# Optimization experiments

Measured on AMD Instinct MI355X. Metric: run time of the kernel, lower is better.

The kernel has to match this reference:

```python
import jax, jax.numpy as jnp
import numpy as np

NA, NW, H = 20000, 100000, 128
DA, DW = 64, 128
E_CR, E_IN, E_CO = 400000, 600000, 300000


def _seg_softmax(logits, seg, n):
    m = jax.ops.segment_max(logits, seg, num_segments=n)
    e = jnp.exp(logits - m[seg])
    s = jax.ops.segment_sum(e, seg, num_segments=n)
    return e / (s[seg] + 1e-16)


def _gat(x_src, x_dst, edge, W, b, a_s, a_d):
    # PyG GATConv, heads=1, concat=False, shared lin for src/dst, add_self_loops=True
    n_src, n_dst = x_src.shape[0], x_dst.shape[0]
    loops = jnp.arange(min(n_src, n_dst), dtype=edge.dtype)
    src = jnp.concatenate([edge[0], loops])
    dst = jnp.concatenate([edge[1], loops])
    hs = x_src @ W            # [n_src, H]
    hd = x_dst @ W            # [n_dst, H]
    logit = jax.nn.leaky_relu((hs @ a_s)[src] + (hd @ a_d)[dst], 0.2)
    alpha = _seg_softmax(logit, dst, n_dst)          # softmax over in-neighborhoods
    out = jax.ops.segment_sum(alpha[:, None] * hs[src], dst, num_segments=n_dst)
    return out + b


def _mlp2(x, w1, b1, w2, b2):
    return jax.nn.relu(x @ w1 + b1) @ w2 + b2


def setup_inputs() -> dict:
    key = jax.random.key(0)
    ks = iter(jax.random.split(key, 40))

    def p(shape, scale=0.1):
        return jax.random.normal(next(ks), shape, jnp.float32) * scale

    def edges(n_src, n_dst, E):
        s = jax.random.randint(next(ks), (E,), 0, n_src, dtype=jnp.int32)
        d = jax.random.randint(next(ks), (E,), 0, n_dst, dtype=jnp.int32)
        d = jnp.where(s == d, (d + 1) % n_dst, d)  # keep input loop-free (PyG strips them)
        return jnp.stack([s, d])

    e_creates = edges(NA, NW, E_CR)
    inp = {
        'artist_feat': jax.random.normal(next(ks), (NA, DA), jnp.float32),
        'work_feat': jax.random.normal(next(ks), (NW, DW), jnp.float32),
        'a_w1': p((DA, H)), 'a_b1': jnp.zeros(H, jnp.float32),
        'a_w2': p((H, H)), 'a_b2': jnp.zeros(H, jnp.float32),
        'w_w1': p((DW, H)), 'w_b1': jnp.zeros(H, jnp.float32),
        'w_w2': p((H, H)), 'w_b2': jnp.zeros(H, jnp.float32),
        'cr_W': p((H, H)), 'cr_b': jnp.zeros(H, jnp.float32), 'cr_as': p((H,)), 'cr_ad': p((H,)),
        'in_W': p((H, H)), 'in_b': jnp.zeros(H, jnp.float32), 'in_as': p((H,)), 'in_ad': p((H,)),
        'co_W': p((H, H)), 'co_b': jnp.zeros(H, jnp.float32), 'co_as': p((H,)), 'co_ad': p((H,)),
        'p_w1': p((2 * H, 256)), 'p_b1': jnp.zeros(256, jnp.float32),
        'p_w2': p((256, 128)), 'p_b2': jnp.zeros(128, jnp.float32),
        'p_w3': p((128, 1)), 'p_b3': jnp.zeros(1, jnp.float32),
        'e_creates': e_creates,
        'e_created_by': jnp.flip(e_creates, axis=0),  # reverse relation [work, artist]
        'e_infl': edges(NW, NW, E_IN),
        'e_collab': edges(NA, NA, E_CO),
    }
    return inp


def reference(artist_feat, work_feat,
              a_w1, a_b1, a_w2, a_b2,
              w_w1, w_b1, w_w2, w_b2,
              cr_W, cr_b, cr_as, cr_ad,
              in_W, in_b, in_as, in_ad,
              co_W, co_b, co_as, co_ad,
              p_w1, p_b1, p_w2, p_b2, p_w3, p_b3,
              e_creates, e_created_by, e_infl, e_collab):
    ax = _mlp2(artist_feat, a_w1, a_b1, a_w2, a_b2)      # [NA, H]
    wx = _mlp2(work_feat, w_w1, w_b1, w_w2, w_b2)        # [NW, H]
    wx = jax.nn.elu(_gat(ax, wx, e_creates, cr_W, cr_b, cr_as, cr_ad))
    wx = jax.nn.elu(_gat(wx, wx, e_infl, in_W, in_b, in_as, in_ad))
    au = _gat(wx, ax, e_created_by, cr_W, cr_b, cr_as, cr_ad)  # no elu (matches source)
    ac = jax.nn.elu(_gat(au, au, e_collab, co_W, co_b, co_as, co_ad))
    comb = jnp.concatenate([au, ac], axis=1)             # [NA, 2H]
    h = jax.nn.relu(comb @ p_w1 + p_b1)                  # dropout is identity in eval
    h = jax.nn.relu(h @ p_w2 + p_b2)
    return (h @ p_w3 + p_b3).squeeze()
```

## Files before the change

### kernel.cpp

```cpp
#include <hip/hip_runtime.h>
#include <hip/hip_bf16.h>
#include <cstddef>

#define NA 20000
#define NW 100000
#define HH 128
#define DA 64
#define E_CR 400000
#define E_IN 600000
#define E_CO 300000

#define ROW1 0
#define ROW2 (NW)
#define ROW3 (2 * NW)
#define ROW4 (2 * NW + NA)
#define NTOT (2 * NW + 2 * NA)
#define T1 (E_CR + NA)
#define T2 (E_IN + NW)
#define T3 (E_CR + NA)
#define T4 (E_CO + NA)
#define ETOT (T1 + T2 + T3 + T4)
#define CAPW 40
#define CAPA 88

typedef short v8s __attribute__((ext_vector_type(8)));
typedef float v4f __attribute__((ext_vector_type(4)));

constexpr int PSLOT = 2 * 128 * 264;

__device__ inline short f2bf(float x) {
    union { float f; unsigned u; } c; c.f = x;
    unsigned r = c.u + 0x7fff + ((c.u >> 16) & 1);
    return (short)(r >> 16);
}
__device__ inline float bf2f(short s) {
    union { unsigned u; float f; } c; c.u = ((unsigned)(unsigned short)s) << 16;
    return c.f;
}
__device__ inline float bfu2f(unsigned short s) {
    union { unsigned u; float f; } c; c.u = ((unsigned)s) << 16;
    return c.f;
}

__device__ inline void split8(const float* xv, v8s& h, v8s& l) {
#pragma unroll
    for (int p = 0; p < 4; ++p) {
        float2 xf; xf.x = xv[2 * p]; xf.y = xv[2 * p + 1];
        __hip_bfloat162 hb = __float22bfloat162_rn(xf);
        float2 hf = __bfloat1622float2(hb);
        float2 lf; lf.x = xf.x - hf.x; lf.y = xf.y - hf.y;
        __hip_bfloat162 lb = __float22bfloat162_rn(lf);
        union { __hip_bfloat162 b; short2 s; } uh, ul;
        uh.b = hb; ul.b = lb;
        h[2 * p] = uh.s.x; h[2 * p + 1] = uh.s.y;
        l[2 * p] = ul.s.x; l[2 * p + 1] = ul.s.y;
    }
}

struct PrepDesc { const float* src; int ldw; int K; };
struct PrepArgs { PrepDesc d[10]; const float* wvW; const float* wvA; float* vd; };

__global__ __launch_bounds__(256) void k_prep(PrepArgs a, short* __restrict__ out) {
    if (blockIdx.x == 10 * 128) {
        __shared__ float sa[HH];
        int t = threadIdx.x;
        if (t < HH) sa[t] = a.wvA[t];
        __syncthreads();
        if (t < HH) {
            float s = 0.f;
            for (int jj = 0; jj < HH; ++jj) s += a.wvW[(size_t)t * HH + jj] * sa[jj];
            a.vd[t] = s;
        }
        return;
    }
    int m = blockIdx.x >> 7;
    int e = (blockIdx.x & 127) * 256 + threadIdx.x;
    PrepDesc dd = a.d[m];
    int K = dd.K;
    int KP = (K <= 128) ? K + 8 : K;
    if (e >= K * 128) return;
    int n = e & 127, k = e >> 7;
    float x = dd.src[(size_t)k * dd.ldw + n];
    short h = f2bf(x);
    short l = f2bf(x - bf2f(h));
    short* base = out + (size_t)m * PSLOT;
    base[n * KP + k] = h;
    base[128 * KP + n * KP + k] = l;
}

template<int K, int ACT, int NSS, int ST, int LDSB, int OBF, int DUAL>
__global__ __launch_bounds__(256, 2) void k_mfma(
    const float* __restrict__ X, int ldx,
    const short* __restrict__ Wp,
    const float* __restrict__ bias,
    float* __restrict__ Y, int ldy, int M,
    const float* __restrict__ v1, float* __restrict__ ss1,
    const float* __restrict__ v2, float* __restrict__ ss2,
    const float* __restrict__ sb)
{
    constexpr int KF = K / 32;
    constexpr int KP = LDSB ? K + 8 : K;
    __shared__ short Bs[LDSB ? 2 * 128 * (K + 8) : 8];
    const int tid = threadIdx.x;
    const int wave = tid >> 6, lane = tid & 63;
    const int l15 = lane & 15, quad = lane >> 4;
    int bid = blockIdx.x;
    if (DUAL) {
        int g0 = gridDim.x >> 1;
        if (bid >= g0) { bid -= g0; Wp += PSLOT; bias += 128; Y += 128; }
    }
    const int wrow = bid * 128 + wave * 32;

    if (LDSB) {
        const float4* src = (const float4*)Wp;
        float4* dst = (float4*)Bs;
        constexpr int total = 2 * 128 * KP / 8;
        for (int i = tid; i < total; i += 256) dst[i] = src[i];
    }

    v4f acc[2][8];
#pragma unroll
    for (int rf = 0; rf < 2; ++rf)
#pragma unroll
        for (int cf = 0; cf < 8; ++cf) acc[rf][cf] = (v4f){0.f, 0.f, 0.f, 0.f};

    if (LDSB) {
        v8s ah[2][KF], al[2][KF];
#pragma unroll
        for (int rf = 0; rf < 2; ++rf) {
            int r = wrow + rf * 16 + l15; if (r >= M) r = M - 1;
            const float* xp = X + (size_t)r * ldx + quad * 8;
#pragma unroll
            for (int kf = 0; kf < KF; ++kf) {
                float xv[8];
                *(float4*)&xv[0] = *(const float4*)(xp + kf * 32);
                *(float4*)&xv[4] = *(const float4*)(xp + kf * 32 + 4);
                split8(xv, ah[rf][kf], al[rf][kf]);
            }
        }
        __syncthreads();
#pragma unroll
        for (int kf = 0; kf < KF; ++kf) {
#pragma unroll
            for (int cf = 0; cf < 8; ++cf) {
                const short* bp = &Bs[(cf * 16 + l15) * KP + kf * 32 + quad * 8];
                v8s bh = *(const v8s*)bp;
                v8s bl = *(const v8s*)(bp + 128 * KP);
#pragma unroll
                for (int rf = 0; rf < 2; ++rf) {
                    acc[rf][cf] = __builtin_amdgcn_mfma_f32_16x16x32_bf16(al[rf][kf], bh, acc[rf][cf], 0, 0, 0);
                    acc[rf][cf] = __builtin_amdgcn_mfma_f32_16x16x32_bf16(ah[rf][kf], bl, acc[rf][cf], 0, 0, 0);
                    acc[rf][cf] = __builtin_amdgcn_mfma_f32_16x16x32_bf16(ah[rf][kf], bh, acc[rf][cf], 0, 0, 0);
                }
            }
        }
    } else {
        for (int kf = 0; kf < KF; ++kf) {
            v8s ah[2], al[2];
#pragma unroll
            for (int rf = 0; rf < 2; ++rf) {
                int r = wrow + rf * 16 + l15; if (r >= M) r = M - 1;
                const float* xp = X + (size_t)r * ldx + kf * 32 + quad * 8;
                float xv[8];
                *(float4*)&xv[0] = *(const float4*)xp;
                *(float4*)&xv[4] = *(const float4*)(xp + 4);
                split8(xv, ah[rf], al[rf]);
            }
#pragma unroll
            for (int cf = 0; cf < 8; ++cf) {
                const short* bp = Wp + (size_t)(cf * 16 + l15) * K + kf * 32 + quad * 8;
                v8s bh = *(const v8s*)bp;
                v8s bl = *(const v8s*)(bp + 128 * KP);
#pragma unroll
                for (int rf = 0; rf < 2; ++rf) {
                    acc[rf][cf] = __builtin_amdgcn_mfma_f32_16x16x32_bf16(al[rf], bh, acc[rf][cf], 0, 0, 0);
                    acc[rf][cf] = __builtin_amdgcn_mfma_f32_16x16x32_bf16(ah[rf], bl, acc[rf][cf], 0, 0, 0);
                    acc[rf][cf] = __builtin_amdgcn_mfma_f32_16x16x32_bf16(ah[rf], bh, acc[rf][cf], 0, 0, 0);
                }
            }
        }
    }

    float bv[8], v1c[8], v2c[8];
#pragma unroll
    for (int cf = 0; cf < 8; ++cf) {
        int col = cf * 16 + l15;
        bv[cf] = bias ? bias[col] : 0.f;
        if (NSS >= 1) v1c[cf] = v1[col];
        if (NSS >= 2) v2c[cf] = v2[col];
    }
    float sbv = (NSS >= 1 && sb) ? sb[0] : 0.f;

#pragma unroll
    for (int rf = 0; rf < 2; ++rf) {
#pragma unroll
        for (int reg = 0; reg < 4; ++reg) {
            int r = wrow + rf * 16 + quad * 4 + reg;
            if (r >= M) continue;
            float p1 = 0.f, p2 = 0.f;
#pragma unroll
            for (int cf = 0; cf < 8; ++cf) {
                float o = acc[rf][cf][reg] + bv[cf];
                if (ACT == 1) o = o > 0.f ? o : 0.f;
                if (NSS >= 1) p1 = fmaf(o, v1c[cf], p1);
                if (NSS >= 2) p2 = fmaf(o, v2c[cf], p2);
                if (ST) {
                    if (OBF) ((unsigned short*)Y)[(size_t)r * ldy + cf * 16 + l15] = (unsigned short)f2bf(o);
                    else     Y[(size_t)r * ldy + cf * 16 + l15] = o;
                }
            }
            if (NSS >= 1) {
#pragma unroll
                for (int w = 1; w < 16; w <<= 1) {
                    p1 += __shfl_xor(p1, w, 64);
                    if (NSS >= 2) p2 += __shfl_xor(p2, w, 64);
                }
                if (l15 == 0) {
                    ss1[r] = p1 + sbv;
                    if (NSS >= 2) ss2[r] = p2;
                }
            }
        }
    }
}

struct EdgeSets { const int* e[4]; int E[4]; int row[4]; int cum[5]; int* pad[4]; int cap[4]; };

__global__ __launch_bounds__(256) void k_append(EdgeSets es, int* __restrict__ deg)
{
    int b0 = blockIdx.x * 1024 + threadIdx.x;
    int s[4], d[4], g[4]; bool ok[4];
#pragma unroll
    for (int u = 0; u < 4; ++u) {
        int i = b0 + u * 256;
        ok[u] = i < es.cum[4];
        s[u] = 0; d[u] = 0; g[u] = 0;
        if (ok[u]) {
            int gi = (i >= es.cum[1]) + (i >= es.cum[2]) + (i >= es.cum[3]);
            int t = i - es.cum[gi];
            int E = es.E[gi];
            if (t < E) { s[u] = es.e[gi][t]; d[u] = es.e[gi][E + t]; }
            else       { s[u] = t - E;       d[u] = t - E; }
            g[u] = gi;
        }
    }
    int p[4];
#pragma unroll
    for (int u = 0; u < 4; ++u) if (ok[u]) p[u] = atomicAdd(&deg[es.row[g[u]] + d[u]], 1);
#pragma unroll
    for (int u = 0; u < 4; ++u)
        if (ok[u] && p[u] < es.cap[g[u]])
            es.pad[g[u]][(size_t)d[u] * es.cap[g[u]] + p[u]] = s[u];
}

template<int ELU, int U, int CAP>
__global__ __launch_bounds__(256) void k_aggregate(
    const int* __restrict__ deg, const int* __restrict__ esp,
    const unsigned short* __restrict__ hs, const float* __restrict__ ss,
    const float* __restrict__ sd, const float* __restrict__ bias,
    float* __restrict__ out, int ldy, int n)
{
    int lane = threadIdx.x & 63;
    int wv = threadIdx.x >> 6;
    int d = blockIdx.x * 4 + wv;
    if (d >= n) return;
    int half = lane >> 5;
    int col = (lane & 31) * 4;
    const int* row = esp + (size_t)d * CAP;
    int i1 = deg[d]; if (i1 > CAP) i1 = CAP;
    float sdv = sd[d];
    float den = 0.f;
    float ax = 0.f, ay = 0.f, az = 0.f, aw = 0.f;
    int i = 0;
    for (; i + 2 * U <= i1; i += 2 * U) {
        int s[U]; ushort4 h[U]; float sv[U];
#pragma unroll
        for (int u = 0; u < U; ++u) s[u] = row[i + 2 * u + half];
#pragma unroll
        for (int u = 0; u < U; ++u) h[u] = *(const ushort4*)(hs + (size_t)s[u] * HH + col);
#pragma unroll
        for (int u = 0; u < U; ++u) sv[u] = ss[s[u]];
#pragma unroll
        for (int u = 0; u < U; ++u) {
            float l = sv[u] + sdv;
            l = l < 0.f ? 0.2f * l : l;
            float e = __expf(l);
            den += e;
            ax = fmaf(e, bfu2f(h[u].x), ax);
            ay = fmaf(e, bfu2f(h[u].y), ay);
            az = fmaf(e, bfu2f(h[u].z), az);
            aw = fmaf(e, bfu2f(h[u].w), aw);
        }
    }
    if (i < i1) {
        int s[U]; ushort4 h[U]; float sv[U]; bool act[U];
#pragma unroll
        for (int u = 0; u < U; ++u) {
            int idx = i + 2 * u + half;
            act[u] = idx < i1;
            s[u] = row[act[u] ? idx : (i1 - 1)];
        }
#pragma unroll
        for (int u = 0; u < U; ++u) h[u] = *(const ushort4*)(hs + (size_t)s[u] * HH + col);
#pragma unroll
        for (int u = 0; u < U; ++u) sv[u] = ss[s[u]];
#pragma unroll
        for (int u = 0; u < U; ++u) {
            float l = sv[u] + sdv;
            l = l < 0.f ? 0.2f * l : l;
            float e = act[u] ? __expf(l) : 0.f;
            den += e;
            ax = fmaf(e, bfu2f(h[u].x), ax);
            ay = fmaf(e, bfu2f(h[u].y), ay);
            az = fmaf(e, bfu2f(h[u].z), az);
            aw = fmaf(e, bfu2f(h[u].w), aw);
        }
    }
    den += __shfl_xor(den, 32, 64);
    ax += __shfl_xor(ax, 32, 64);
    ay += __shfl_xor(ay, 32, 64);
    az += __shfl_xor(az, 32, 64);
    aw += __shfl_xor(aw, 32, 64);
    if (half == 0) {
        float4 b = *(const float4*)(bias + col);
        float inv = 1.f / (den + 1e-16f);
        float o0 = ax * inv + b.x;
        float o1 = ay * inv + b.y;
        float o2 = az * inv + b.z;
        float o3 = aw * inv + b.w;
        if (ELU) {
            o0 = o0 > 0.f ? o0 : expm1f(o0);
            o1 = o1 > 0.f ? o1 : expm1f(o1);
            o2 = o2 > 0.f ? o2 : expm1f(o2);
            o3 = o3 > 0.f ? o3 : expm1f(o3);
        }
        *(float4*)(out + (size_t)d * ldy + col) = make_float4(o0, o1, o2, o3);
    }
}

extern "C" void kernel_launch(void* const* d_in, const int* in_sizes, int n_in,
                              void* d_out, int out_size, void* d_ws, size_t ws_size,
                              hipStream_t stream)
{
    const float* artist = (const float*)d_in[0];
    const float* workf  = (const float*)d_in[1];
    const float* a_w1 = (const float*)d_in[2];  const float* a_b1 = (const float*)d_in[3];
    const float* a_w2 = (const float*)d_in[4];  const float* a_b2 = (const float*)d_in[5];
    const float* w_w1 = (const float*)d_in[6];  const float* w_b1 = (const float*)d_in[7];
    const float* w_w2 = (const float*)d_in[8];  const float* w_b2 = (const float*)d_in[9];
    const float* cr_W = (const float*)d_in[10]; const float* cr_b = (const float*)d_in[11];
    const float* cr_as = (const float*)d_in[12]; const float* cr_ad = (const float*)d_in[13];
    const float* in_W = (const float*)d_in[14]; const float* in_b = (const float*)d_in[15];
    const float* in_as = (const float*)d_in[16]; const float* in_ad = (const float*)d_in[17];
    const float* co_W = (const float*)d_in[18]; const float* co_b = (const float*)d_in[19];
    const float* co_as = (const float*)d_in[20]; const float* co_ad = (const float*)d_in[21];
    const float* p_w1 = (const float*)d_in[22]; const float* p_b1 = (const float*)d_in[23];
    const float* p_w2 = (const float*)d_in[24]; const float* p_b2 = (const float*)d_in[25];
    const float* p_w3 = (const float*)d_in[26]; const float* p_b3 = (const float*)d_in[27];
    const int* e_cr = (const int*)d_in[28];
    const int* e_cb = (const int*)d_in[29];
    const int* e_in = (const int*)d_in[30];
    const int* e_co = (const int*)d_in[31];

    char* wsp = (char*)d_ws;
    size_t off = 0;
    auto alloc = [&](size_t bytes) -> void* {
        void* p = wsp + off;
        off += (bytes + 255) / 256 * 256;
        return p;
    };
    float* ax   = (float*)alloc((size_t)NA * HH * 4);
    float* wx   = (float*)alloc((size_t)NW * HH * 4);
    float* hs   = (float*)alloc((size_t)NW * HH * 4);
    unsigned short* hsb = (unsigned short*)alloc((size_t)NW * HH * 2);
    float* comb = (float*)alloc((size_t)NA * 256 * 4);
    float* ss1 = (float*)alloc((size_t)NA * 4);
    float* sd1 = (float*)alloc((size_t)NW * 4);
    float* ss2 = (float*)alloc((size_t)NW * 4);
    float* sd2 = (float*)alloc((size_t)NW * 4);
    float* ss3 = (float*)alloc((size_t)NW * 4);
    float* sd3 = (float*)alloc((size_t)NA * 4);
    float* ss4 = (float*)alloc((size_t)NA * 4);
    float* sd4 = (float*)alloc((size_t)NA * 4);
    float* vd  = (float*)alloc(HH * 4);
    int* deg   = (int*)alloc((size_t)NTOT * 4);
    int* pad1  = (int*)alloc((size_t)NW * CAPW * 4);
    int* pad2  = (int*)alloc((size_t)NW * CAPW * 4);
    int* pad3  = (int*)alloc((size_t)NA * CAPA * 4);
    int* pad4  = (int*)alloc((size_t)NA * CAPA * 4);
    short* preW = (short*)alloc((size_t)10 * PSLOT * 2);
    (void)ws_size; (void)in_sizes; (void)n_in; (void)out_size;

    auto pre = [&](int m) { return preW + (size_t)m * PSLOT; };
    auto gg = [](int M) { return (M + 127) / 128; };
    const float* nf = nullptr;
    float* nfm = nullptr;

    EdgeSets es;
    es.e[0] = e_cr; es.e[1] = e_in; es.e[2] = e_cb; es.e[3] = e_co;
    es.E[0] = E_CR; es.E[1] = E_IN; es.E[2] = E_CR; es.E[3] = E_CO;
    es.row[0] = ROW1; es.row[1] = ROW2; es.row[2] = ROW3; es.row[3] = ROW4;
    es.cum[0] = 0; es.cum[1] = T1; es.cum[2] = T1 + T2; es.cum[3] = T1 + T2 + T3; es.cum[4] = ETOT;
    es.pad[0] = pad1; es.pad[1] = pad2; es.pad[2] = pad3; es.pad[3] = pad4;
    es.cap[0] = CAPW; es.cap[1] = CAPW; es.cap[2] = CAPA; es.cap[3] = CAPA;
    (void)hipMemsetAsync(deg, 0, (size_t)NTOT * 4, stream);
    k_append<<<(ETOT + 1023) / 1024, 256, 0, stream>>>(es, deg);

    PrepArgs pa;
    pa.d[0] = {a_w1, HH, DA};
    pa.d[1] = {a_w2, HH, HH};
    pa.d[2] = {w_w1, HH, HH};
    pa.d[3] = {w_w2, HH, HH};
    pa.d[4] = {cr_W, HH, HH};
    pa.d[5] = {in_W, HH, HH};
    pa.d[6] = {co_W, HH, HH};
    pa.d[7] = {p_w1, 256, 256};
    pa.d[8] = {p_w1 + 128, 256, 256};
    pa.d[9] = {p_w2, HH, 256};
    pa.wvW = cr_W; pa.wvA = cr_ad; pa.vd = vd;
    k_prep<<<10 * 128 + 1, 256, 0, stream>>>(pa, preW);

    k_mfma<DA, 1, 0, 1, 1, 0, 0><<<gg(NA), 256, 0, stream>>>(artist, DA, pre(0), a_b1, hs, HH, NA, nf, nfm, nf, nfm, nf);
    k_mfma<HH, 0, 1, 1, 1, 0, 0><<<gg(NA), 256, 0, stream>>>(hs, HH, pre(1), a_b2, ax, HH, NA, vd, sd3, nf, nfm, nf);
    k_mfma<HH, 1, 0, 1, 1, 0, 0><<<gg(NW), 256, 0, stream>>>(workf, HH, pre(2), w_b1, hs, HH, NW, nf, nfm, nf, nfm, nf);
    k_mfma<HH, 0, 1, 1, 1, 0, 0><<<gg(NW), 256, 0, stream>>>(hs, HH, pre(3), w_b2, wx, HH, NW, vd, sd1, nf, nfm, nf);

    k_mfma<HH, 0, 1, 1, 1, 1, 0><<<gg(NA), 256, 0, stream>>>(ax, HH, pre(4), nullptr, (float*)hsb, HH, NA, cr_as, ss1, nf, nfm, nf);
    k_aggregate<1, 2, CAPW><<<(NW + 3) / 4, 256, 0, stream>>>(deg + ROW1, pad1, hsb, ss1, sd1, cr_b, wx, HH, NW);

    k_mfma<HH, 0, 2, 1, 1, 1, 0><<<gg(NW), 256, 0, stream>>>(wx, HH, pre(5), nullptr, (float*)hsb, HH, NW, in_as, ss2, in_ad, sd2, nf);
    k_aggregate<1, 2, CAPW><<<(NW + 3) / 4, 256, 0, stream>>>(deg + ROW2, pad2, hsb, ss2, sd2, in_b, wx, HH, NW);

    k_mfma<HH, 0, 1, 1, 1, 1, 0><<<gg(NW), 256, 0, stream>>>(wx, HH, pre(4), nullptr, (float*)hsb, HH, NW, cr_as, ss3, nf, nfm, nf);
    k_aggregate<0, 4, CAPA><<<(NA + 3) / 4, 256, 0, stream>>>(deg + ROW3, pad3, hsb, ss3, sd3, cr_b, comb, 256, NA);

    k_mfma<HH, 0, 2, 1, 1, 1, 0><<<gg(NA), 256, 0, stream>>>(comb, 256, pre(6), nullptr, (float*)hsb, HH, NA, co_as, ss4, co_ad, sd4, nf);
    k_aggregate<1, 4, CAPA><<<(NA + 3) / 4, 256, 0, stream>>>(deg + ROW4, pad4, hsb, ss4, sd4, co_b, comb + 128, 256, NA);

    float* h1 = hs;
    k_mfma<256, 1, 0, 1, 0, 0, 1><<<2 * gg(NA), 256, 0, stream>>>(comb, 256, pre(7), p_b1, h1, 256, NA, nf, nfm, nf, nfm, nf);
    k_mfma<256, 1, 1, 0, 0, 0, 0><<<gg(NA), 256, 0, stream>>>(h1, 256, pre(9), p_b2, nfm, 0, NA, p_w3, (float*)d_out, nf, nfm, p_b3);
}
```

Before: 634.9 us.

## Merge prep with edge append, batch independent GEMMs, handle self-loops inline

Merges the weight-prep and edge-append kernels into one launch. Pairs independent artist and work MLP GEMMs into single launches through a new dual-config MFMA kernel. Self-loop edges are no longer written to the padded adjacency lists; the aggregate kernel adds the self-loop term directly for d < loopn. This cuts launch count, atomics and padded-list slots, but the generic kernel reads its config at runtime and adds a branch to aggregate.

Result: faster. 617.7 us (-2.7%).

```diff
diff --git a/kernel.cpp b/kernel.cpp
--- a/kernel.cpp
+++ b/kernel.cpp
@@ -15,13 +15,10 @@
 #define ROW3 (2 * NW)
 #define ROW4 (2 * NW + NA)
 #define NTOT (2 * NW + 2 * NA)
-#define T1 (E_CR + NA)
-#define T2 (E_IN + NW)
-#define T3 (E_CR + NA)
-#define T4 (E_CO + NA)
-#define ETOT (T1 + T2 + T3 + T4)
+#define ETOTR (E_CR + E_IN + E_CR + E_CO)
 #define CAPW 40
 #define CAPA 88
+#define NPREP (10 * 128 + 1)
 
 typedef short v8s __attribute__((ext_vector_type(8)));
 typedef float v4f __attribute__((ext_vector_type(4)));
@@ -59,33 +56,61 @@
 
 struct PrepDesc { const float* src; int ldw; int K; };
 struct PrepArgs { PrepDesc d[10]; const float* wvW; const float* wvA; float* vd; };
-
-__global__ __launch_bounds__(256) void k_prep(PrepArgs a, short* __restrict__ out) {
-    if (blockIdx.x == 10 * 128) {
-        __shared__ float sa[HH];
-        int t = threadIdx.x;
-        if (t < HH) sa[t] = a.wvA[t];
-        __syncthreads();
-        if (t < HH) {
-            float s = 0.f;
-            for (int jj = 0; jj < HH; ++jj) s += a.wvW[(size_t)t * HH + jj] * sa[jj];
-            a.vd[t] = s;
-        }
+struct EdgeSets { const int* e[4]; int E[4]; int row[4]; int cum[5]; int* pad[4]; int cap[4]; };
+
+__global__ __launch_bounds__(256) void k_prep_append(PrepArgs a, short* __restrict__ out,
+                                                    EdgeSets es, int* __restrict__ deg)
+{
+    if (blockIdx.x < NPREP) {
+        if (blockIdx.x == NPREP - 1) {
+            __shared__ float sa[HH];
+            int t = threadIdx.x;
+            if (t < HH) sa[t] = a.wvA[t];
+            __syncthreads();
+            if (t < HH) {
+                float s = 0.f;
+                for (int jj = 0; jj < HH; ++jj) s += a.wvW[(size_t)t * HH + jj] * sa[jj];
+                a.vd[t] = s;
+            }
+            return;
+        }
+        int m = blockIdx.x >> 7;
+        int e = (blockIdx.x & 127) * 256 + threadIdx.x;
+        PrepDesc dd = a.d[m];
+        int K = dd.K;
+        int KP = (K <= 128) ? K + 8 : K;
+        if (e >= K * 128) return;
+        int n = e & 127, k = e >> 7;
+        float x = dd.src[(size_t)k * dd.ldw + n];
+        short h = f2bf(x);
+        short l = f2bf(x - bf2f(h));
+        short* base = out + (size_t)m * PSLOT;
+        base[n * KP + k] = h;
+        base[128 * KP + n * KP + k] = l;
         return;
     }
-    int m = blockIdx.x >> 7;
-    int e = (blockIdx.x & 127) * 256 + threadIdx.x;
-    PrepDesc dd = a.d[m];
-    int K = dd.K;
-    int KP = (K <= 128) ? K + 8 : K;
-    if (e >= K * 128) return;
-    int n = e & 127, k = e >> 7;
-    float x = dd.src[(size_t)k * dd.ldw + n];
-    short h = f2bf(x);
-    short l = f2bf(x - bf2f(h));
-    short* base = out + (size_t)m * PSLOT;
-    base[n * KP + k] = h;
-    base[128 * KP + n * KP + k] = l;
+    int b0 = (blockIdx.x - NPREP) * 1024 + threadIdx.x;
+    int s[4], d[4], g[4]; bool ok[4];
+#pragma unroll
+    for (int u = 0; u < 4; ++u) {
+        int i = b0 + u * 256;
+        ok[u] = i < es.cum[4];
+        s[u] = 0; d[u] = 0; g[u] = 0;
+        if (ok[u]) {
+            int gi = (i >= es.cum[1]) + (i >= es.cum[2]) + (i >= es.cum[3]);
+            int t = i - es.cum[gi];
+            s[u] = es.e[gi][t];
+            d[u] = es.e[gi][es.E[gi] + t];
+            g[u] = gi;
+        }
+    }
+    int p[4];
+#pragma unroll
+    for (int u = 0; u < 4; ++u) if (ok[u]) p[u] = atomicAdd(&deg[es.row[g[u]] + d[u]], 1);
+#pragma unroll
+    for (int u = 0; u < 4; ++u)
+        if (ok[u] && p[u] < es.cap[g[u]])
+            es.pad[g[u]][(size_t)d[u] * es.cap[g[u]] + p[u]] = s[u];
 }
 
 template<int K, int ACT, int NSS, int ST, int LDSB, int OBF, int DUAL>
@@ -224,33 +249,110 @@
     }
 }
 
-struct EdgeSets { const int* e[4]; int E[4]; int row[4]; int cum[5]; int* pad[4]; int cap[4]; };
-
-__global__ __launch_bounds__(256) void k_append(EdgeSets es, int* __restrict__ deg)
+struct MfmaCfg {
+    const float* X; int ldx;
+    const short* Wp;
+    const float* bias;
+    float* Y; int ldy; int M;
+    int act, nss, obf;
+    const float* v1; float* ss1;
+    const float* v2; float* ss2;
+    int nblocks;
+};
+
+__global__ __launch_bounds__(256, 2) void k_mfma2(MfmaCfg c0, MfmaCfg c1)
 {
-    int b0 = blockIdx.x * 1024 + threadIdx.x;
-    int s[4], d[4], g[4]; bool ok[4];
-#pragma unroll
-    for (int u = 0; u < 4; ++u) {
-        int i = b0 + u * 256;
-        ok[u] = i < es.cum[4];
-        s[u] = 0; d[u] = 0; g[u] = 0;
-        if (ok[u]) {
-            int gi = (i >= es.cum[1]) + (i >= es.cum[2]) + (i >= es.cum[3]);
-            int t = i - es.cum[gi];
-            int E = es.E[gi];
-            if (t < E) { s[u] = es.e[gi][t]; d[u] = es.e[gi][E + t]; }
-            else       { s[u] = t - E;       d[u] = t - E; }
-            g[u] = gi;
-        }
-    }
-    int p[4];
-#pragma unroll
-    for (int u = 0; u < 4; ++u) if (ok[u]) p[u] = atomicAdd(&deg[es.row[g[u]] + d[u]], 1);
-#pragma unroll
-    for (int u = 0; u < 4; ++u)
-        if (ok[u] && p[u] < es.cap[g[u]])
-            es.pad[g[u]][(size_t)d[u] * es.cap[g[u]] + p[u]] = s[u];
+    constexpr int K = 128, KF = 4, KP = 136;
+    __shared__ short Bs[2 * 128 * KP];
+    const bool first = blockIdx.x < c0.nblocks;
+    const MfmaCfg& c = first ? c0 : c1;
+    const int bid = first ? blockIdx.x : blockIdx.x - c0.nblocks;
+    const int tid = threadIdx.x;
+    const int wave = tid >> 6, lane = tid & 63;
+    const int l15 = lane & 15, quad = lane >> 4;
+    const int wrow = bid * 128 + wave * 32;
+
+    {
+        const float4* src = (const float4*)c.Wp;
+        float4* dst = (float4*)Bs;
+        constexpr int total = 2 * 128 * KP / 8;
+        for (int i = tid; i < total; i += 256) dst[i] = src[i];
+    }
+
+    v4f acc[2][8];
+#pragma unroll
+    for (int rf = 0; rf < 2; ++rf)
+#pragma unroll
+        for (int cf = 0; cf < 8; ++cf) acc[rf][cf] = (v4f){0.f, 0.f, 0.f, 0.f};
+
+    v8s ah[2][KF], al[2][KF];
+#pragma unroll
+    for (int rf = 0; rf < 2; ++rf) {
+        int r = wrow + rf * 16 + l15; if (r >= c.M) r = c.M - 1;
+        const float* xp = c.X + (size_t)r * c.ldx + quad * 8;
+#pragma unroll
+        for (int kf = 0; kf < KF; ++kf) {
+            float xv[8];
+            *(float4*)&xv[0] = *(const float4*)(xp + kf * 32);
+            *(float4*)&xv[4] = *(const float4*)(xp + kf * 32 + 4);
+            split8(xv, ah[rf][kf], al[rf][kf]);
+        }
+    }
+    __syncthreads();
+#pragma unroll
+    for (int kf = 0; kf < KF; ++kf) {
+#pragma unroll
+        for (int cf = 0; cf < 8; ++cf) {
+            const short* bp = &Bs[(cf * 16 + l15) * KP + kf * 32 + quad * 8];
+            v8s bh = *(const v8s*)bp;
+            v8s bl = *(const v8s*)(bp + 128 * KP);
+#pragma unroll
+            for (int rf = 0; rf < 2; ++rf) {
+                acc[rf][cf] = __builtin_amdgcn_mfma_f32_16x16x32_bf16(al[rf][kf], bh, acc[rf][cf], 0, 0, 0);
+                acc[rf][cf] = __builtin_amdgcn_mfma_f32_16x16x32_bf16(ah[rf][kf], bl, acc[rf][cf], 0, 0, 0);
+                acc[rf][cf] = __builtin_amdgcn_mfma_f32_16x16x32_bf16(ah[rf][kf], bh, acc[rf][cf], 0, 0, 0);
+            }
+        }
+    }
+
+    float bv[8], v1c[8], v2c[8];
+#pragma unroll
+    for (int cf = 0; cf < 8; ++cf) {
+        int col = cf * 16 + l15;
+        bv[cf] = c.bias ? c.bias[col] : 0.f;
+        v1c[cf] = (c.nss >= 1) ? c.v1[col] : 0.f;
+        v2c[cf] = (c.nss >= 2) ? c.v2[col] : 0.f;
+    }
+
+#pragma unroll
+    for (int rf = 0; rf < 2; ++rf) {
+#pragma unroll
+        for (int reg = 0; reg < 4; ++reg) {
+            int r = wrow + rf * 16 + quad * 4 + reg;
+            if (r >= c.M) continue;
+            float p1 = 0.f, p2 = 0.f;
+#pragma unroll
+            for (int cf = 0; cf < 8; ++cf) {
+                float o = acc[rf][cf][reg] + bv[cf];
+                if (c.act) o = o > 0.f ? o : 0.f;
+                p1 = fmaf(o, v1c[cf], p1);
+                p2 = fmaf(o, v2c[cf], p2);
+                if (c.obf) ((unsigned short*)c.Y)[(size_t)r * c.ldy + cf * 16 + l15] = (unsigned short)f2bf(o);
+                else       c.Y[(size_t)r * c.ldy + cf * 16 + l15] = o;
+            }
+            if (c.nss >= 1) {
+#pragma unroll
+                for (int w = 1; w < 16; w <<= 1) {
+                    p1 += __shfl_xor(p1, w, 64);
+                    p2 += __shfl_xor(p2, w, 64);
+                }
+                if (l15 == 0) {
+                    c.ss1[r] = p1;
+                    if (c.nss >= 2) c.ss2[r] = p2;
+                }
+            }
+        }
+    }
 }
 
 template<int ELU, int U, int CAP>
@@ -258,7 +360,7 @@
     const int* __restrict__ deg, const int* __restrict__ esp,
     const unsigned short* __restrict__ hs, const float* __restrict__ ss,
     const float* __restrict__ sd, const float* __restrict__ bias,
-    float* __restrict__ out, int ldy, int n)
+    float* __restrict__ out, int ldy, int n, int loopn)
 {
     int lane = threadIdx.x & 63;
     int wv = threadIdx.x >> 6;
@@ -271,6 +373,17 @@
     float sdv = sd[d];
     float den = 0.f;
     float ax = 0.f, ay = 0.f, az = 0.f, aw = 0.f;
+    if (half == 0 && d < loopn) {
+        ushort4 h = *(const ushort4*)(hs + (size_t)d * HH + col);
+        float l = ss[d] + sdv;
+        l = l < 0.f ? 0.2f * l : l;
+        float e = __expf(l);
+        den += e;
+        ax = fmaf(e, bfu2f(h.x), ax);
+        ay = fmaf(e, bfu2f(h.y), ay);
+        az = fmaf(e, bfu2f(h.z), az);
+        aw = fmaf(e, bfu2f(h.w), aw);
+    }
     int i = 0;
     for (; i + 2 * U <= i1; i += 2 * U) {
         int s[U]; ushort4 h[U]; float sv[U];
@@ -370,6 +483,7 @@
         return p;
     };
     float* ax   = (float*)alloc((size_t)NA * HH * 4);
+    float* hsA  = (float*)alloc((size_t)NA * HH * 4);
     float* wx   = (float*)alloc((size_t)NW * HH * 4);
     float* hs   = (float*)alloc((size_t)NW * HH * 4);
     unsigned short* hsb = (unsigned short*)alloc((size_t)NW * HH * 2);
@@ -396,16 +510,6 @@
     const float* nf = nullptr;
     float* nfm = nullptr;
 
-    EdgeSets es;
-    es.e[0] = e_cr; es.e[1] = e_in; es.e[2] = e_cb; es.e[3] = e_co;
-    es.E[0] = E_CR; es.E[1] = E_IN; es.E[2] = E_CR; es.E[3] = E_CO;
-    es.row[0] = ROW1; es.row[1] = ROW2; es.row[2] = ROW3; es.row[3] = ROW4;
-    es.cum[0] = 0; es.cum[1] = T1; es.cum[2] = T1 + T2; es.cum[3] = T1 + T2 + T3; es.cum[4] = ETOT;
-    es.pad[0] = pad1; es.pad[1] = pad2; es.pad[2] = pad3; es.pad[3] = pad4;
-    es.cap[0] = CAPW; es.cap[1] = CAPW; es.cap[2] = CAPA; es.cap[3] = CAPA;
-    (void)hipMemsetAsync(deg, 0, (size_t)NTOT * 4, stream);
-    k_append<<<(ETOT + 1023) / 1024, 256, 0, stream>>>(es, deg);
-
     PrepArgs pa;
     pa.d[0] = {a_w1, HH, DA};
     pa.d[1] = {a_w2, HH, HH};
@@ -418,24 +522,43 @@
     pa.d[8] = {p_w1 + 128, 256, 256};
     pa.d[9] = {p_w2, HH, 256};
     pa.wvW = cr_W; pa.wvA = cr_ad; pa.vd = vd;
-    k_prep<<<10 * 128 + 1, 256, 0, stream>>>(pa, preW);
-
-    k_mfma<DA, 1, 0, 1, 1, 0, 0><<<gg(NA), 256, 0, stream>>>(artist, DA, pre(0), a_b1, hs, HH, NA, nf, nfm, nf, nfm, nf);
-    k_mfma<HH, 0, 1, 1, 1, 0, 0><<<gg(NA), 256, 0, stream>>>(hs, HH, pre(1), a_b2, ax, HH, NA, vd, sd3, nf, nfm, nf);
-    k_mfma<HH, 1, 0, 1, 1, 0, 0><<<gg(NW), 256, 0, stream>>>(workf, HH, pre(2), w_b1, hs, HH, NW, nf, nfm, nf, nfm, nf);
-    k_mfma<HH, 0, 1, 1, 1, 0, 0><<<gg(NW), 256, 0, stream>>>(hs, HH, pre(3), w_b2, wx, HH, NW, vd, sd1, nf, nfm, nf);
-
-    k_mfma<HH, 0, 1, 1, 1, 1, 0><<<gg(NA), 256, 0, stream>>>(ax, HH, pre(4), nullptr, (float*)hsb, HH, NA, cr_as, ss1, nf, nfm, nf);
-    k_aggregate<1, 2, CAPW><<<(NW + 3) / 4, 256, 0, stream>>>(deg + ROW1, pad1, hsb, ss1, sd1, cr_b, wx, HH, NW);
+
+    EdgeSets es;
+    es.e[0] = e_cr; es.e[1] = e_in; es.e[2] = e_cb; es.e[3] = e_co;
+    es.E[0] = E_CR; es.E[1] = E_IN; es.E[2] = E_CR; es.E[3] = E_CO;
+    es.row[0] = ROW1; es.row[1] = ROW2; es.row[2] = ROW3; es.row[3] = ROW4;
+    es.cum[0] = 0; es.cum[1] = E_CR; es.cum[2] = E_CR + E_IN;
+    es.cum[3] = E_CR + E_IN + E_CR; es.cum[4] = ETOTR;
+    es.pad[0] = pad1; es.pad[1] = pad2; es.pad[2] = pad3; es.pad[3] = pad4;
+    es.cap[0] = CAPW; es.cap[1] = CAPW; es.cap[2] = CAPA; es.cap[3] = CAPA;
+
+    (void)hipMemsetAsync(deg, 0, (size_t)NTOT * 4, stream);
+    int nApp = (ETOTR + 1023) / 1024;
+    k_prep_append<<<NPREP + nApp, 256, 0, stream>>>(pa, preW, es, deg);
+
+    k_mfma<DA, 1, 0, 1, 1, 0, 0><<<gg(NA), 256, 0, stream>>>(artist, DA, pre(0), a_b1, hsA, HH, NA, nf, nfm, nf, nfm, nf);
+
+    {
+        MfmaCfg c0 = {workf, HH, pre(2), w_b1, hs, HH, NW, 1, 0, 0, nf, nfm, nf, nfm, gg(NW)};
+        MfmaCfg c1 = {hsA, HH, pre(1), a_b2, ax, HH, NA, 0, 1, 0, vd, sd3, nf, nfm, gg(NA)};
+        k_mfma2<<<gg(NW) + gg(NA), 256, 0, stream>>>(c0, c1);
+    }
+    {
+        MfmaCfg c0 = {hs, HH, pre(3), w_b2, wx, HH, NW, 0, 1, 0, vd, sd1, nf, nfm, gg(NW)};
+        MfmaCfg c1 = {ax, HH, pre(4), nullptr, (float*)hsb, HH, NA, 0, 1, 1, cr_as, ss1, nf, nfm, gg(NA)};
+        k_mfma2<<<gg(NW) + gg(NA), 256, 0, stream>>>(c0, c1);
+    }
+
+    k_aggregate<1, 2, CAPW><<<(NW + 3) / 4, 256, 0, stream>>>(deg + ROW1, pad1, hsb, ss1, sd1, cr_b, wx, HH, NW, NA);
 
     k_mfma<HH, 0, 2, 1, 1, 1, 0><<<gg(NW), 256, 0, stream>>>(wx, HH, pre(5), nullptr, (float*)hsb, HH, NW, in_as, ss2, in_ad, sd2, nf);
-    k_aggregate<1, 2, CAPW><<<(NW + 3) / 4, 256, 0, stream>>>(deg + ROW2, pad2, hsb, ss2, sd2, in_b, wx, HH, NW);
+    k_aggregate<1, 2, CAPW><<<(NW + 3) / 4, 256, 0, stream>>>(deg + ROW2, pad2, hsb, ss2, sd2, in_b, wx, HH, NW, NW);
 
     k_mfma<HH, 0, 1, 1, 1, 1, 0><<<gg(NW), 256, 0, stream>>>(wx, HH, pre(4), nullptr, (float*)hsb, HH, NW, cr_as, ss3, nf, nfm, nf);
-    k_aggregate<0, 4, CAPA><<<(NA + 3) / 4, 256, 0, stream>>>(deg + ROW3, pad3, hsb, ss3, sd3, cr_b, comb, 256, NA);
+    k_aggregate<0, 4, CAPA><<<(NA + 3) / 4, 256, 0, stream>>>(deg + ROW3, pad3, hsb, ss3, sd3, cr_b, comb, 256, NA, NA);
 
     k_mfma<HH, 0, 2, 1, 1, 1, 0><<<gg(NA), 256, 0, stream>>>(comb, 256, pre(6), nullptr, (float*)hsb, HH, NA, co_as, ss4, co_ad, sd4, nf);
-    k_aggregate<1, 4, CAPA><<<(NA + 3) / 4, 256, 0, stream>>>(deg + ROW4, pad4, hsb, ss4, sd4, co_b, comb + 128, 256, NA);
+    k_aggregate<1, 4, CAPA><<<(NA + 3) / 4, 256, 0, stream>>>(deg + ROW4, pad4, hsb, ss4, sd4, co_b, comb + 128, 256, NA, NA);
 
     float* h1 = hs;
     k_mfma<256, 1, 0, 1, 0, 0, 1><<<2 * gg(NA), 256, 0, stream>>>(comb, 256, pre(7), p_b1, h1, 256, NA, nf, nfm, nf, nfm, nf);
```
